# Optimization experiments

Hardware: AMD Instinct MI355X
Metric: run time of the kernel (lower is better)

Reference implementation:

```python
import jax, jax.numpy as jnp
import numpy as np
import math

H = 256; W = 256
NUM_CURVES = 256
NUM_SAMPLES = 32
NUM_BEZIERS = 2
BDEG = 5            # Bernstein degree used by the module (bezier_degree+1)
CTRL_STRIDE = 5     # bezier_degree+1; segments share endpoints, wrap (closed curve)
N_CTRL = NUM_BEZIERS * CTRL_STRIDE   # 10 control points per closed curve
PIX_CHUNK = 512
CHOLESKY_BOUND = jnp.array([0.5, 0.0, 0.5], jnp.float32)


def _bernstein():
    # t in linspace(0.007, 0.993, S) exactly as _update_bernstein_cache
    t = jnp.linspace(0.007, 0.993, NUM_SAMPLES)
    i = jnp.arange(BDEG + 1, dtype=jnp.float32)
    comb = jnp.array([math.comb(BDEG, k) for k in range(BDEG + 1)], jnp.float32)
    return comb * (t[:, None] ** i) * ((1.0 - t[:, None]) ** (BDEG - i))  # [S, BDEG+1]


def _render(control_points, features_dc, cholesky, opacity, depth, background):
    Bmat = _bernstein()
    # closed curve: segment k uses control points (k*5 + j) mod 10, j=0..5
    seg_idx = (jnp.arange(NUM_BEZIERS)[:, None] * CTRL_STRIDE
               + jnp.arange(BDEG + 1)[None, :]) % N_CTRL          # [K, 6]
    seg_ctrl = control_points[:, seg_idx]                          # [N, K, 6, 2]
    pts = jnp.einsum('sj,nkjd->nksd', Bmat, seg_ctrl)              # [N, K, S, 2]
    pts = pts.reshape(NUM_CURVES, -1, 2)                           # [N, Gper, 2]
    gper = pts.shape[1]

    # normalized [-1,1] -> pixel coords
    means = (jnp.tanh(pts) * 0.5 + 0.5) * jnp.array([W, H], jnp.float32)
    means = means.reshape(-1, 2)                                   # [G, 2]

    # 2x2 covariance from lower-triangular Cholesky (per curve)
    c = cholesky + CHOLESKY_BOUND[None, :]                         # l11, l21, l22
    s00 = c[:, 0] ** 2
    s01 = c[:, 0] * c[:, 1]
    s11 = c[:, 1] ** 2 + c[:, 2] ** 2
    det = s00 * s11 - s01 ** 2
    conic = jnp.stack([s11 / det, -s01 / det, s00 / det], -1)      # [N, 3]

    rep = lambda a: jnp.repeat(a, gper, axis=0)
    conic_g = rep(conic)                                           # [G, 3]
    color_g = rep(jax.nn.sigmoid(features_dc))                     # [G, 3]
    alpha_g = rep(jax.nn.sigmoid(opacity))[:, 0]                   # [G]
    depth_g = rep(depth)[:, 0]                                     # [G]

    order = jnp.argsort(depth_g)                                   # front-to-back
    means_s = means[order]
    conic_s = conic_g[order]
    color_s = color_g[order]
    alpha_s = alpha_g[order]

    ys, xs = jnp.meshgrid(jnp.arange(H, dtype=jnp.float32) + 0.5,
                          jnp.arange(W, dtype=jnp.float32) + 0.5, indexing='ij')
    pix = jnp.stack([xs.ravel(), ys.ravel()], -1).reshape(-1, PIX_CHUNK, 2)

    @jax.checkpoint
    def render_chunk(p):                                           # [C,2] -> [C,3]
        dx = p[:, None, 0] - means_s[None, :, 0]
        dy = p[:, None, 1] - means_s[None, :, 1]
        power = (-0.5 * (conic_s[None, :, 0] * dx * dx
                         + conic_s[None, :, 2] * dy * dy)
                 - conic_s[None, :, 1] * dx * dy)
        a = jnp.clip(alpha_s[None, :] * jnp.exp(power), 0.0, 0.999)
        logT = jnp.cumsum(jnp.log1p(-a), axis=1)
        t_excl = jnp.exp(logT - jnp.log1p(-a))   # transmittance before each splat
        rgb = (a * t_excl) @ color_s             # [C, 3]
        return rgb + jnp.exp(logT[:, -1:]) * background[None, :]

    img = jax.lax.map(render_chunk, pix)                           # [P/C, C, 3]
    return jnp.clip(img.reshape(H, W, 3), 0.0, 1.0)


def setup_inputs() -> dict:
    key = jax.random.key(0)
    k1, k2, k3, k4 = jax.random.split(key, 4)
    return {
        "control_points": jax.random.normal(k1, (NUM_CURVES, N_CTRL, 2), jnp.float32),
        "features_dc": jax.random.uniform(k2, (NUM_CURVES, 3), jnp.float32),
        "cholesky": jax.random.uniform(k3, (NUM_CURVES, 3), jnp.float32),
        "opacity": jnp.ones((NUM_CURVES, 1), jnp.float32),
        "depth": jax.random.uniform(k4, (NUM_CURVES, 1), jnp.float32),
        "background": jnp.ones((3,), jnp.float32),
    }


def reference(control_points, features_dc, cholesky, opacity, depth, background):
    return _render(control_points, features_dc, cholesky, opacity, depth, background)
```

## Files before the change

### kernel.cpp

```cpp
#include <hip/hip_runtime.h>
#include <math.h>

#define NCURVES   256
#define GPER      64
#define NUM_G     (NCURVES*GPER)
#define IMG_W     256
#define IMG_H     256
#define TILE      16
#define TILES_X   (IMG_W/TILE)
#define TILES_Y   (IMG_H/TILE)
#define NTILES    (TILES_X*TILES_Y)
#define REC_F     12
#define SEGS      16
#define GSEG      (NUM_G/SEGS)
#define NSUB      (GSEG/256)

#define A_MIN     3.0e-6f
#define P_CUT     (-12.6f)
#define T_EPS     1.0e-5f

__global__ __launch_bounds__(GPER)
void prep(const float* __restrict__ ctrl,
          const float* __restrict__ features,
          const float* __restrict__ cholesky,
          const float* __restrict__ opacity,
          const float* __restrict__ depth,
          float*       __restrict__ recs,
          unsigned*    __restrict__ bbox)
{
    int c   = blockIdx.x;
    int tid = threadIdx.x;

    float dc = depth[c];
    int r = 0;
    #pragma unroll
    for (int jj = 0; jj < 4; ++jj) {
        int j = tid + jj*64;
        float dj = depth[j];
        r += (dj < dc) || (dj == dc && j < c);
    }
    #pragma unroll
    for (int off = 32; off > 0; off >>= 1) r += __shfl_down(r, off, 64);
    r = __shfl(r, 0, 64);

    float c0 = cholesky[3*c+0] + 0.5f;
    float c1 = cholesky[3*c+1];
    float c2 = cholesky[3*c+2] + 0.5f;
    float s00 = c0*c0;
    float s01 = c0*c1;
    float s11 = c1*c1 + c2*c2;
    float inv = 1.0f / (s00*s11 - s01*s01);
    float A  =  s11*inv;
    float Bc = -s01*inv;
    float Cc =  s00*inv;

    float cr = 1.0f/(1.0f + __expf(-features[3*c+0]));
    float cg = 1.0f/(1.0f + __expf(-features[3*c+1]));
    float cb = 1.0f/(1.0f + __expf(-features[3*c+2]));
    float al = 1.0f/(1.0f + __expf(-opacity[c]));

    float cut = fmaxf(2.0f*(__logf(al) - __logf(A_MIN)), 0.0f);
    float rx = sqrtf(cut * s00);
    float ry = sqrtf(cut * s11);

    int k = tid >> 5;
    int s = tid & 31;
    float t = 0.007f + (float)s * (0.986f/31.0f);
    float u = 1.0f - t;
    float t2=t*t, t3=t2*t, t4=t3*t, t5=t4*t;
    float u2=u*u, u3=u2*u, u4=u3*u, u5=u4*u;
    float w[6] = { u5, 5.0f*t*u4, 10.0f*t2*u3, 10.0f*t3*u2, 5.0f*t4*u, t5 };

    const float* cp = ctrl + c*20;
    float px = 0.0f, py = 0.0f;
    #pragma unroll
    for (int j = 0; j < 6; ++j) {
        int idx = (k*5 + j) % 10;
        px += w[j]*cp[2*idx+0];
        py += w[j]*cp[2*idx+1];
    }
    float mx = (tanhf(px)*0.5f + 0.5f) * (float)IMG_W;
    float my = (tanhf(py)*0.5f + 0.5f) * (float)IMG_H;

    int gi = r*GPER + tid;
    float* o = recs + (size_t)gi*REC_F;
    o[0]=mx; o[1]=my; o[2]=A; o[3]=Bc; o[4]=Cc; o[5]=al;
    o[6]=cr; o[7]=cg; o[8]=cb; o[9]=0.0f; o[10]=0.0f; o[11]=0.0f;

    int tx0 = min(max((int)floorf((mx - rx) * (1.0f/TILE)), 0), TILES_X-1);
    int tx1 = min(max((int)floorf((mx + rx) * (1.0f/TILE)), 0), TILES_X-1);
    int ty0 = min(max((int)floorf((my - ry) * (1.0f/TILE)), 0), TILES_Y-1);
    int ty1 = min(max((int)floorf((my + ry) * (1.0f/TILE)), 0), TILES_Y-1);
    bbox[gi] = (unsigned)tx0 | ((unsigned)ty0<<8) | ((unsigned)tx1<<16) | ((unsigned)ty1<<24);
}

__global__ __launch_bounds__(256)
void render_seg(const float*    __restrict__ recs,
                const unsigned* __restrict__ bbox,
                float4*         __restrict__ partial)
{
    __shared__ float4   data[256][3];
    __shared__ unsigned wcnt[4];

    int tid   = threadIdx.x;
    int seg   = blockIdx.x & (SEGS-1);
    int tile  = blockIdx.x >> 4;
    int tilex = tile & (TILES_X-1);
    int tiley = tile >> 4;
    int X = tilex*TILE + (tid & (TILE-1));
    int Y = tiley*TILE + (tid >> 4);
    float px = (float)X + 0.5f;
    float py = (float)Y + 0.5f;

    int lane = tid & 63;
    int wid  = tid >> 6;
    unsigned long long lmask = (1ull << lane) - 1ull;

    int gbeg = seg * GSEG;

    bool pred[NSUB];
    {
        unsigned bb[NSUB];
        #pragma unroll
        for (int b = 0; b < NSUB; ++b) bb[b] = bbox[gbeg + b*256 + tid];
        #pragma unroll
        for (int b = 0; b < NSUB; ++b) {
            unsigned v = bb[b];
            int tx0 =  v        & 0xff;
            int ty0 = (v >> 8)  & 0xff;
            int tx1 = (v >> 16) & 0xff;
            int ty1 = (v >> 24) & 0xff;
            pred[b] = (tilex >= tx0) & (tilex <= tx1) & (tiley >= ty0) & (tiley <= ty1);
        }
    }

    float T = 1.0f, accr = 0.0f, accg = 0.0f, accb = 0.0f;

    #pragma unroll 1
    for (int b = 0; b < NSUB; ++b) {
        unsigned long long m = __ballot(pred[b] ? 1 : 0);
        if (lane == 0) wcnt[wid] = (unsigned)__popcll(m);

        int nalive = __syncthreads_count(T > T_EPS);
        if (nalive == 0) break;

        unsigned c0 = wcnt[0], c1 = wcnt[1], c2 = wcnt[2], c3 = wcnt[3];
        int total = (int)(c0 + c1 + c2 + c3);
        if (total) {
            if (pred[b]) {
                unsigned woff = (wid > 0 ? c0 : 0u) + (wid > 1 ? c1 : 0u) + (wid > 2 ? c2 : 0u);
                int slot = (int)(woff + (unsigned)__popcll(m & lmask));
                const float4* rp = (const float4*)(recs + (size_t)(gbeg + b*256 + tid)*REC_F);
                float4 d0 = rp[0], d1 = rp[1], d2 = rp[2];
                data[slot][0] = d0;
                data[slot][1] = d1;
                data[slot][2] = d2;
            }
            __syncthreads();

            if (T > T_EPS) {
                for (int j = 0; j < total; ++j) {
                    float4 q0 = data[j][0];
                    float4 q1 = data[j][1];
                    float  cb_ = data[j][2].x;
                    float dx = px - q0.x;
                    float dy = py - q0.y;
                    float p  = -0.5f*(q0.z*dx*dx + q1.x*dy*dy) - q0.w*dx*dy;
                    if (p > P_CUT) {
                        float a = q1.y * __expf(p);
                        a = fminf(a, 0.999f);
                        float wgt = a * T;
                        accr += wgt * q1.z;
                        accg += wgt * q1.w;
                        accb += wgt * cb_;
                        T *= (1.0f - a);
                        if (T < T_EPS) break;
                    }
                }
            }
        }
    }

    partial[(size_t)seg*(IMG_W*IMG_H) + (size_t)Y*IMG_W + X] =
        make_float4(accr, accg, accb, T);
}

__global__ __launch_bounds__(256)
void combine(const float4* __restrict__ partial,
             const float*  __restrict__ background,
             float*        __restrict__ out)
{
    int p = blockIdx.x * 256 + threadIdx.x;

    float accr = 0.0f, accg = 0.0f, accb = 0.0f, T = 1.0f;
    #pragma unroll
    for (int s = 0; s < SEGS; ++s) {
        float4 q = partial[(size_t)s*(IMG_W*IMG_H) + p];
        accr += T * q.x;
        accg += T * q.y;
        accb += T * q.z;
        T    *= q.w;
    }
    float r = fminf(fmaxf(accr + T*background[0], 0.0f), 1.0f);
    float g = fminf(fmaxf(accg + T*background[1], 0.0f), 1.0f);
    float b = fminf(fmaxf(accb + T*background[2], 0.0f), 1.0f);

    size_t oi = (size_t)p*3;
    out[oi+0] = r;
    out[oi+1] = g;
    out[oi+2] = b;
}

extern "C" void kernel_launch(void* const* d_in, const int* in_sizes, int n_in,
                              void* d_out, int out_size, void* d_ws, size_t ws_size,
                              hipStream_t stream)
{
    const float* ctrl       = (const float*)d_in[0];
    const float* features   = (const float*)d_in[1];
    const float* cholesky   = (const float*)d_in[2];
    const float* opacity    = (const float*)d_in[3];
    const float* depth      = (const float*)d_in[4];
    const float* background = (const float*)d_in[5];
    float* out = (float*)d_out;

    char* w = (char*)d_ws;
    float*    recs    = (float*)   (w);
    unsigned* bboxp   = (unsigned*)(w + 786432);
    float4*   partial = (float4*)  (w + 786432 + 65536);

    prep<<<NCURVES, GPER, 0, stream>>>(ctrl, features, cholesky, opacity, depth,
                                       recs, bboxp);
    render_seg<<<SEGS*NTILES, 256, 0, stream>>>(recs, bboxp, partial);
    combine<<<(IMG_W*IMG_H)/256, 256, 0, stream>>>(partial, background, out);
}
```

Before: 92.45 us.

## Render each tile in one block with compacted splat list, drop segment combine

Replaces the 16-way depth-segmented render plus combine pass with one block per tile. Each wave first scans a quarter of all splat bounding boxes and builds a compacted index list in shared memory. The block then streams only the overlapping splats in 256-wide batches and writes final pixels directly. This removes the partial-buffer traffic, the combine launch, and per-batch ballots over empty segments. In exchange the grid drops to 256 blocks, which reduces parallelism, and each block now scans all 16K bboxes serially.

```diff
diff --git a/kernel.cpp b/kernel.cpp
--- a/kernel.cpp
+++ b/kernel.cpp
@@ -11,13 +11,14 @@
 #define TILES_Y   (IMG_H/TILE)
 #define NTILES    (TILES_X*TILES_Y)
 #define REC_F     12
-#define SEGS      16
-#define GSEG      (NUM_G/SEGS)
-#define NSUB      (GSEG/256)
 
 #define A_MIN     3.0e-6f
 #define P_CUT     (-12.6f)
 #define T_EPS     1.0e-5f
+
+#define WAVES     4
+#define GPW       (NUM_G/WAVES)
+#define SCAN_B    16
 
 __global__ __launch_bounds__(GPER)
 void prep(const float* __restrict__ ctrl,
@@ -95,117 +96,107 @@
 }
 
 __global__ __launch_bounds__(256)
-void render_seg(const float*    __restrict__ recs,
-                const unsigned* __restrict__ bbox,
-                float4*         __restrict__ partial)
+void render_tile(const float*    __restrict__ recs,
+                 const unsigned* __restrict__ bbox,
+                 const float*    __restrict__ background,
+                 float*          __restrict__ out)
 {
+    __shared__ unsigned short lst[WAVES][GPW];
     __shared__ float4   data[256][3];
-    __shared__ unsigned wcnt[4];
+    __shared__ unsigned wn[WAVES];
 
     int tid   = threadIdx.x;
-    int seg   = blockIdx.x & (SEGS-1);
-    int tile  = blockIdx.x >> 4;
+    int tile  = blockIdx.x;
     int tilex = tile & (TILES_X-1);
     int tiley = tile >> 4;
-    int X = tilex*TILE + (tid & (TILE-1));
-    int Y = tiley*TILE + (tid >> 4);
-    float px = (float)X + 0.5f;
-    float py = (float)Y + 0.5f;
 
     int lane = tid & 63;
     int wid  = tid >> 6;
     unsigned long long lmask = (1ull << lane) - 1ull;
 
-    int gbeg = seg * GSEG;
-
-    bool pred[NSUB];
-    {
-        unsigned bb[NSUB];
+    int gbase = wid * GPW;
+    int cnt = 0;
+    #pragma unroll 1
+    for (int c = 0; c < GPW; c += 64*SCAN_B) {
+        unsigned v[SCAN_B];
         #pragma unroll
-        for (int b = 0; b < NSUB; ++b) bb[b] = bbox[gbeg + b*256 + tid];
+        for (int u = 0; u < SCAN_B; ++u)
+            v[u] = bbox[gbase + c + u*64 + lane];
         #pragma unroll
-        for (int b = 0; b < NSUB; ++b) {
-            unsigned v = bb[b];
-            int tx0 =  v        & 0xff;
-            int ty0 = (v >> 8)  & 0xff;
-            int tx1 = (v >> 16) & 0xff;
-            int ty1 = (v >> 24) & 0xff;
-            pred[b] = (tilex >= tx0) & (tilex <= tx1) & (tiley >= ty0) & (tiley <= ty1);
+        for (int u = 0; u < SCAN_B; ++u) {
+            unsigned b = v[u];
+            int tx0 =  b        & 0xff;
+            int ty0 = (b >> 8)  & 0xff;
+            int tx1 = (b >> 16) & 0xff;
+            int ty1 = (b >> 24) & 0xff;
+            bool pred = (tilex >= tx0) & (tilex <= tx1) &
+                        (tiley >= ty0) & (tiley <= ty1);
+            unsigned long long m = __ballot(pred ? 1 : 0);
+            if (pred)
+                lst[wid][cnt + (int)__popcll(m & lmask)] =
+                    (unsigned short)(c + u*64 + lane);
+            cnt += (int)__popcll(m);
         }
     }
+    if (lane == 0) wn[wid] = (unsigned)cnt;
+    __syncthreads();
+
+    unsigned n0 = wn[0], n1 = wn[1], n2 = wn[2], n3 = wn[3];
+    int total = (int)(n0 + n1 + n2 + n3);
+
+    float px = (float)(tilex*TILE + (tid & (TILE-1))) + 0.5f;
+    float py = (float)(tiley*TILE + (tid >> 4)) + 0.5f;
 
     float T = 1.0f, accr = 0.0f, accg = 0.0f, accb = 0.0f;
 
     #pragma unroll 1
-    for (int b = 0; b < NSUB; ++b) {
-        unsigned long long m = __ballot(pred[b] ? 1 : 0);
-        if (lane == 0) wcnt[wid] = (unsigned)__popcll(m);
-
+    for (int cb = 0; cb < total; cb += 256) {
+        int k = cb + tid;
+        if (k < total) {
+            unsigned off = (unsigned)k; int w = 0;
+            if (off >= n0) { off -= n0; w = 1;
+              if (off >= n1) { off -= n1; w = 2;
+                if (off >= n2) { off -= n2; w = 3; } } }
+            int gi = w*GPW + (int)lst[w][off];
+            const float4* rp = (const float4*)(recs + (size_t)gi*REC_F);
+            float4 d0 = rp[0], d1 = rp[1], d2 = rp[2];
+            data[tid][0] = d0;
+            data[tid][1] = d1;
+            data[tid][2] = d2;
+        }
         int nalive = __syncthreads_count(T > T_EPS);
         if (nalive == 0) break;
 
-        unsigned c0 = wcnt[0], c1 = wcnt[1], c2 = wcnt[2], c3 = wcnt[3];
-        int total = (int)(c0 + c1 + c2 + c3);
-        if (total) {
-            if (pred[b]) {
-                unsigned woff = (wid > 0 ? c0 : 0u) + (wid > 1 ? c1 : 0u) + (wid > 2 ? c2 : 0u);
-                int slot = (int)(woff + (unsigned)__popcll(m & lmask));
-                const float4* rp = (const float4*)(recs + (size_t)(gbeg + b*256 + tid)*REC_F);
-                float4 d0 = rp[0], d1 = rp[1], d2 = rp[2];
-                data[slot][0] = d0;
-                data[slot][1] = d1;
-                data[slot][2] = d2;
-            }
-            __syncthreads();
-
-            if (T > T_EPS) {
-                for (int j = 0; j < total; ++j) {
-                    float4 q0 = data[j][0];
-                    float4 q1 = data[j][1];
-                    float  cb_ = data[j][2].x;
-                    float dx = px - q0.x;
-                    float dy = py - q0.y;
-                    float p  = -0.5f*(q0.z*dx*dx + q1.x*dy*dy) - q0.w*dx*dy;
-                    if (p > P_CUT) {
-                        float a = q1.y * __expf(p);
-                        a = fminf(a, 0.999f);
-                        float wgt = a * T;
-                        accr += wgt * q1.z;
-                        accg += wgt * q1.w;
-                        accb += wgt * cb_;
-                        T *= (1.0f - a);
-                        if (T < T_EPS) break;
-                    }
+        int n = min(256, total - cb);
+        if (T > T_EPS) {
+            for (int j = 0; j < n; ++j) {
+                float4 q0 = data[j][0];
+                float4 q1 = data[j][1];
+                float  cb_ = data[j][2].x;
+                float dx = px - q0.x;
+                float dy = py - q0.y;
+                float p  = -0.5f*(q0.z*dx*dx + q1.x*dy*dy) - q0.w*dx*dy;
+                if (p > P_CUT) {
+                    float a = fminf(q1.y * __expf(p), 0.999f);
+                    float wgt = a * T;
+                    accr += wgt * q1.z;
+                    accg += wgt * q1.w;
+                    accb += wgt * cb_;
+                    T *= (1.0f - a);
+                    if (T < T_EPS) break;
                 }
             }
         }
-    }
-
-    partial[(size_t)seg*(IMG_W*IMG_H) + (size_t)Y*IMG_W + X] =
-        make_float4(accr, accg, accb, T);
-}
-
-__global__ __launch_bounds__(256)
-void combine(const float4* __restrict__ partial,
-             const float*  __restrict__ background,
-             float*        __restrict__ out)
-{
-    int p = blockIdx.x * 256 + threadIdx.x;
-
-    float accr = 0.0f, accg = 0.0f, accb = 0.0f, T = 1.0f;
-    #pragma unroll
-    for (int s = 0; s < SEGS; ++s) {
-        float4 q = partial[(size_t)s*(IMG_W*IMG_H) + p];
-        accr += T * q.x;
-        accg += T * q.y;
-        accb += T * q.z;
-        T    *= q.w;
-    }
+        __syncthreads();
+    }
+
     float r = fminf(fmaxf(accr + T*background[0], 0.0f), 1.0f);
     float g = fminf(fmaxf(accg + T*background[1], 0.0f), 1.0f);
     float b = fminf(fmaxf(accb + T*background[2], 0.0f), 1.0f);
 
-    size_t oi = (size_t)p*3;
+    int X = tilex*TILE + (tid & (TILE-1));
+    int Y = tiley*TILE + (tid >> 4);
+    size_t oi = ((size_t)Y*IMG_W + X)*3;
     out[oi+0] = r;
     out[oi+1] = g;
     out[oi+2] = b;
@@ -224,12 +215,10 @@
     float* out = (float*)d_out;
 
     char* w = (char*)d_ws;
-    float*    recs    = (float*)   (w);
-    unsigned* bboxp   = (unsigned*)(w + 786432);
-    float4*   partial = (float4*)  (w + 786432 + 65536);
+    float*    recs  = (float*)   (w);
+    unsigned* bboxp = (unsigned*)(w + 786432);
 
     prep<<<NCURVES, GPER, 0, stream>>>(ctrl, features, cholesky, opacity, depth,
                                        recs, bboxp);
-    render_seg<<<SEGS*NTILES, 256, 0, stream>>>(recs, bboxp, partial);
-    combine<<<(IMG_W*IMG_H)/256, 256, 0, stream>>>(partial, background, out);
+    render_tile<<<NTILES, 256, 0, stream>>>(recs, bboxp, background, out);
 }
```

Result: slower. 121.2 us (+31.1%).

## Compact per-tile index list once, read splat records from global in render loop

Applied to the files above, without the earlier changes.

The render kernel now culls all splats of a segment up front and builds one compacted list of 16-bit indices in shared memory. Each pixel thread then walks that list and loads records directly from global/L1 instead of staging batches through shared memory with per-batch barriers. The record shrinks from 12 to 8 floats by packing colors as fp16, and the segment count drops from 16 to 8. The early-termination transmittance check is removed, so every pixel visits every listed splat, and colors lose some precision.

```diff
diff --git a/kernel.cpp b/kernel.cpp
--- a/kernel.cpp
+++ b/kernel.cpp
@@ -1,4 +1,5 @@
 #include <hip/hip_runtime.h>
+#include <hip/hip_fp16.h>
 #include <math.h>
 
 #define NCURVES   256
@@ -10,14 +11,14 @@
 #define TILES_X   (IMG_W/TILE)
 #define TILES_Y   (IMG_H/TILE)
 #define NTILES    (TILES_X*TILES_Y)
-#define REC_F     12
-#define SEGS      16
-#define GSEG      (NUM_G/SEGS)
-#define NSUB      (GSEG/256)
+#define REC_F     8
 
 #define A_MIN     3.0e-6f
 #define P_CUT     (-12.6f)
-#define T_EPS     1.0e-5f
+
+#define SEGS      8
+#define GSEG      (NUM_G/SEGS)
+#define GWAVE     (GSEG/4)
 
 __global__ __launch_bounds__(GPER)
 void prep(const float* __restrict__ ctrl,
@@ -83,9 +84,14 @@
     float my = (tanhf(py)*0.5f + 0.5f) * (float)IMG_H;
 
     int gi = r*GPER + tid;
-    float* o = recs + (size_t)gi*REC_F;
-    o[0]=mx; o[1]=my; o[2]=A; o[3]=Bc; o[4]=Cc; o[5]=al;
-    o[6]=cr; o[7]=cg; o[8]=cb; o[9]=0.0f; o[10]=0.0f; o[11]=0.0f;
+
+    unsigned rg  = (unsigned)__half_as_ushort(__float2half_rn(cr))
+                 | ((unsigned)__half_as_ushort(__float2half_rn(cg)) << 16);
+    unsigned cbp = (unsigned)__half_as_ushort(__float2half_rn(cb));
+
+    float4* o4 = (float4*)(recs + (size_t)gi*REC_F);
+    o4[0] = make_float4(mx, my, A, Bc);
+    o4[1] = make_float4(Cc, al, __uint_as_float(rg), __uint_as_float(cbp));
 
     int tx0 = min(max((int)floorf((mx - rx) * (1.0f/TILE)), 0), TILES_X-1);
     int tx1 = min(max((int)floorf((mx + rx) * (1.0f/TILE)), 0), TILES_X-1);
@@ -95,92 +101,92 @@
 }
 
 __global__ __launch_bounds__(256)
-void render_seg(const float*    __restrict__ recs,
-                const unsigned* __restrict__ bbox,
-                float4*         __restrict__ partial)
-{
-    __shared__ float4   data[256][3];
-    __shared__ unsigned wcnt[4];
+void render8(const float*    __restrict__ recs,
+             const unsigned* __restrict__ bbox,
+             float4*         __restrict__ partial)
+{
+    __shared__ unsigned short flat[GSEG];
+    __shared__ unsigned       wn[4];
 
     int tid   = threadIdx.x;
     int seg   = blockIdx.x & (SEGS-1);
-    int tile  = blockIdx.x >> 4;
+    int tile  = blockIdx.x >> 3;
     int tilex = tile & (TILES_X-1);
     int tiley = tile >> 4;
-    int X = tilex*TILE + (tid & (TILE-1));
-    int Y = tiley*TILE + (tid >> 4);
-    float px = (float)X + 0.5f;
-    float py = (float)Y + 0.5f;
 
     int lane = tid & 63;
     int wid  = tid >> 6;
     unsigned long long lmask = (1ull << lane) - 1ull;
 
-    int gbeg = seg * GSEG;
-
-    bool pred[NSUB];
+    int sbase = seg * GSEG;
+    int gwave = wid * GWAVE;
+
+    bool pr[8];
+    int cnt = 0;
     {
-        unsigned bb[NSUB];
+        unsigned bb[8];
         #pragma unroll
-        for (int b = 0; b < NSUB; ++b) bb[b] = bbox[gbeg + b*256 + tid];
+        for (int u = 0; u < 8; ++u)
+            bb[u] = bbox[sbase + gwave + u*64 + lane];
         #pragma unroll
-        for (int b = 0; b < NSUB; ++b) {
-            unsigned v = bb[b];
-            int tx0 =  v        & 0xff;
-            int ty0 = (v >> 8)  & 0xff;
-            int tx1 = (v >> 16) & 0xff;
-            int ty1 = (v >> 24) & 0xff;
-            pred[b] = (tilex >= tx0) & (tilex <= tx1) & (tiley >= ty0) & (tiley <= ty1);
+        for (int u = 0; u < 8; ++u) {
+            unsigned b = bb[u];
+            pr[u] = (tilex >= (int)( b        & 0xff)) &
+                    (tilex <= (int)((b >> 16) & 0xff)) &
+                    (tiley >= (int)((b >>  8) & 0xff)) &
+                    (tiley <= (int)((b >> 24) & 0xff));
+            cnt += (int)__popcll(__ballot(pr[u] ? 1 : 0));
         }
     }
+    if (lane == 0) wn[wid] = (unsigned)cnt;
+    __syncthreads();
+
+    unsigned p1 = wn[0], p2 = p1 + wn[1], p3 = p2 + wn[2];
+    int total = (int)(p3 + wn[3]);
+
+    if (total) {
+        unsigned base = (wid == 0) ? 0u : (wid == 1) ? p1 : (wid == 2) ? p2 : p3;
+        int off = 0;
+        #pragma unroll
+        for (int u = 0; u < 8; ++u) {
+            unsigned long long m = __ballot(pr[u] ? 1 : 0);
+            if (pr[u])
+                flat[base + off + (int)__popcll(m & lmask)] =
+                    (unsigned short)(gwave + u*64 + lane);
+            off += (int)__popcll(m);
+        }
+    }
+    __syncthreads();
+
+    int ix = tid & (TILE-1);
+    int iy = tid >> 4;
+    float pxf = (float)(tilex*TILE + ix) + 0.5f;
+    float pyf = (float)(tiley*TILE + iy) + 0.5f;
 
     float T = 1.0f, accr = 0.0f, accg = 0.0f, accb = 0.0f;
 
-    #pragma unroll 1
-    for (int b = 0; b < NSUB; ++b) {
-        unsigned long long m = __ballot(pred[b] ? 1 : 0);
-        if (lane == 0) wcnt[wid] = (unsigned)__popcll(m);
-
-        int nalive = __syncthreads_count(T > T_EPS);
-        if (nalive == 0) break;
-
-        unsigned c0 = wcnt[0], c1 = wcnt[1], c2 = wcnt[2], c3 = wcnt[3];
-        int total = (int)(c0 + c1 + c2 + c3);
-        if (total) {
-            if (pred[b]) {
-                unsigned woff = (wid > 0 ? c0 : 0u) + (wid > 1 ? c1 : 0u) + (wid > 2 ? c2 : 0u);
-                int slot = (int)(woff + (unsigned)__popcll(m & lmask));
-                const float4* rp = (const float4*)(recs + (size_t)(gbeg + b*256 + tid)*REC_F);
-                float4 d0 = rp[0], d1 = rp[1], d2 = rp[2];
-                data[slot][0] = d0;
-                data[slot][1] = d1;
-                data[slot][2] = d2;
-            }
-            __syncthreads();
-
-            if (T > T_EPS) {
-                for (int j = 0; j < total; ++j) {
-                    float4 q0 = data[j][0];
-                    float4 q1 = data[j][1];
-                    float  cb_ = data[j][2].x;
-                    float dx = px - q0.x;
-                    float dy = py - q0.y;
-                    float p  = -0.5f*(q0.z*dx*dx + q1.x*dy*dy) - q0.w*dx*dy;
-                    if (p > P_CUT) {
-                        float a = q1.y * __expf(p);
-                        a = fminf(a, 0.999f);
-                        float wgt = a * T;
-                        accr += wgt * q1.z;
-                        accg += wgt * q1.w;
-                        accb += wgt * cb_;
-                        T *= (1.0f - a);
-                        if (T < T_EPS) break;
-                    }
-                }
-            }
+    #pragma unroll 2
+    for (int j = 0; j < total; ++j) {
+        int gl = (int)flat[j];
+        const float4* rp = (const float4*)(recs + (size_t)(sbase + gl)*REC_F);
+        float4 r0 = rp[0];
+        float4 r1 = rp[1];
+        float dx = pxf - r0.x;
+        float dy = pyf - r0.y;
+        float p  = -0.5f*(r0.z*dx*dx + r1.x*dy*dy) - r0.w*dx*dy;
+        if (p > P_CUT) {
+            float a = fminf(r1.y * __expf(p), 0.999f);
+            float wgt = a * T;
+            unsigned rg = __float_as_uint(r1.z);
+            accr += wgt * __half2float(__ushort_as_half((unsigned short)(rg & 0xffff)));
+            accg += wgt * __half2float(__ushort_as_half((unsigned short)(rg >> 16)));
+            accb += wgt * __half2float(__ushort_as_half((unsigned short)__float_as_uint(r1.w)));
+            T *= (1.0f - a);
         }
     }
 
+    int X = tilex*TILE + ix;
+    int Y = tiley*TILE + iy;
     partial[(size_t)seg*(IMG_W*IMG_H) + (size_t)Y*IMG_W + X] =
         make_float4(accr, accg, accb, T);
 }
@@ -225,11 +231,11 @@
 
     char* w = (char*)d_ws;
     float*    recs    = (float*)   (w);
-    unsigned* bboxp   = (unsigned*)(w + 786432);
-    float4*   partial = (float4*)  (w + 786432 + 65536);
+    unsigned* bboxp   = (unsigned*)(w + 524288);
+    float4*   partial = (float4*)  (w + 524288 + 65536);
 
     prep<<<NCURVES, GPER, 0, stream>>>(ctrl, features, cholesky, opacity, depth,
                                        recs, bboxp);
-    render_seg<<<SEGS*NTILES, 256, 0, stream>>>(recs, bboxp, partial);
+    render8<<<NTILES*SEGS, 256, 0, stream>>>(recs, bboxp, partial);
     combine<<<(IMG_W*IMG_H)/256, 256, 0, stream>>>(partial, background, out);
 }
```

After: 84.32 us. -8.8%, faster.
